# Kernel tuning notes

Measured on AMD Instinct MI355X. Metric: run time of the kernel, lower is better.

The kernel has to match this reference:

```python
import jax, jax.numpy as jnp
import numpy as np

NUM_HEADS = 8
HIDDEN_DIM = 256
QUERY_DIM = 256
HEAD_DIM = HIDDEN_DIM // NUM_HEADS
NORM_FACT = float(HIDDEN_DIM / NUM_HEADS) ** (-0.5)


def setup_inputs() -> dict:
    key = jax.random.key(0)
    k1, k2, k3, k4, k5 = jax.random.split(key, 5)
    B, Q, H, W = 16, 100, 64, 64
    q = jax.random.normal(k1, (B, Q, QUERY_DIM), dtype=jnp.float32)
    k = jax.random.normal(k2, (B, QUERY_DIM, H, W), dtype=jnp.float32)
    mask = jax.random.randint(k3, (B, H, W), 0, 2).astype(jnp.bool_)
    # xavier_uniform for [hidden, query] linear weights
    limit = float(np.sqrt(6.0 / (HIDDEN_DIM + QUERY_DIM)))
    Wq = jax.random.uniform(k4, (HIDDEN_DIM, QUERY_DIM), minval=-limit, maxval=limit, dtype=jnp.float32)
    Wk = jax.random.uniform(k5, (HIDDEN_DIM, QUERY_DIM), minval=-limit, maxval=limit, dtype=jnp.float32)
    bq = jnp.zeros((HIDDEN_DIM,), dtype=jnp.float32)
    bk = jnp.zeros((HIDDEN_DIM,), dtype=jnp.float32)
    return {"q": q, "k": k, "Wq": Wq, "bq": bq, "Wk": Wk, "bk": bk, "mask": mask}


def reference(q, k, Wq, bq, Wk, bk, mask):
    B, Q, _ = q.shape
    _, C, H, W = k.shape
    # q projection: [B, Q, hidden]
    qp = jnp.einsum('bqc,hc->bqh', q, Wq) + bq
    # k projection via 1x1 conv == channelwise linear: [B, hidden, H, W]
    kp = jnp.einsum('bchw,oc->bohw', k, Wk) + bk[None, :, None, None]
    # split heads: qh [B,Q,nh,hd], kh [B,nh,hd,H,W]
    qh = qp.reshape(B, Q, NUM_HEADS, HEAD_DIM)
    kh = kp.reshape(B, NUM_HEADS, HEAD_DIM, H, W)
    # scores [B,Q,nh,H,W]
    weights = jnp.einsum('bqnd,bndhw->bqnhw', qh, kh) * NORM_FACT
    # masked fill: mask [B,H,W] -> broadcast over (Q, heads)
    weights = jnp.where(mask[:, None, None, :, :], -jnp.inf, weights)
    # softmax jointly over (heads, H, W), as in torch flatten(2)
    flat = weights.reshape(B, Q, NUM_HEADS * H * W)
    flat = jax.nn.softmax(flat, axis=-1)
    return flat.reshape(B, Q, NUM_HEADS, H, W)
```

## Files before the change

kernel.cpp:

```cpp
#include <hip/hip_runtime.h>
#include <hip/hip_bf16.h>
#include <math.h>

#define BB 16
#define QQ 100
#define NH 8
#define HWN 4096
#define NORM_FACT 0.17677669529663687f
#define QPAD 112

typedef short bf16x8_t __attribute__((ext_vector_type(8)));
typedef float f32x4_t  __attribute__((ext_vector_type(4)));

__device__ __forceinline__ unsigned short bf16bits(float f) {
    __hip_bfloat16 h = __float2bfloat16(f);
    return __builtin_bit_cast(unsigned short, h);
}
__device__ __forceinline__ float bf16tof(unsigned short u) {
    union { unsigned int i; float f; } x; x.i = (unsigned int)u << 16; return x.f;
}

__global__ void k_prep(const float* __restrict__ Wq, const float* __restrict__ Wk,
                       float* __restrict__ WqT, unsigned short* __restrict__ Wkbf) {
    int idx = blockIdx.x;
    int h = threadIdx.x;
    if (idx < 256) {
        WqT[idx * 256 + h] = Wq[h * 256 + idx];
    } else {
        int r = idx - 256;
        Wkbf[r * 256 + h] = bf16bits(Wk[r * 256 + h]);
    }
}

__global__ __launch_bounds__(256) void k_qproj(const float* __restrict__ q,
                                               const float* __restrict__ WqT,
                                               const float* __restrict__ bq,
                                               unsigned short* __restrict__ qphi,
                                               unsigned short* __restrict__ qplo) {
    int blk = blockIdx.x;
    int b = blk / 28, q0 = (blk % 28) * 4;
    int h = threadIdx.x;
    size_t obase = ((size_t)b * QPAD + q0) * 256 + h;
    if (q0 >= QQ) {
#pragma unroll
        for (int i = 0; i < 4; ++i) { qphi[obase + i * 256] = 0; qplo[obase + i * 256] = 0; }
        return;
    }
    __shared__ float qsh[4][256];
    int ibase = (b * QQ + q0) * 256;
#pragma unroll
    for (int i = 0; i < 4; ++i) qsh[i][h] = q[ibase + i * 256 + h];
    __syncthreads();
    float bias = bq[h];
    float a0 = bias, a1 = bias, a2 = bias, a3 = bias;
    for (int c = 0; c < 256; ++c) {
        float wv = WqT[c * 256 + h];
        a0 = fmaf(qsh[0][c], wv, a0);
        a1 = fmaf(qsh[1][c], wv, a1);
        a2 = fmaf(qsh[2][c], wv, a2);
        a3 = fmaf(qsh[3][c], wv, a3);
    }
    float a[4] = {a0 * NORM_FACT, a1 * NORM_FACT, a2 * NORM_FACT, a3 * NORM_FACT};
#pragma unroll
    for (int i = 0; i < 4; ++i) {
        unsigned short hi = bf16bits(a[i]);
        qphi[obase + i * 256] = hi;
        qplo[obase + i * 256] = bf16bits(a[i] - bf16tof(hi));
    }
}

__global__ __launch_bounds__(512) void k_kproj3(const float* __restrict__ k,
                                                const unsigned short* __restrict__ Wkbf,
                                                const float* __restrict__ bk,
                                                unsigned short* __restrict__ kpT) {
    int b = blockIdx.y;
    int hwblk = blockIdx.x * 64;
    int t = threadIdx.x;
    int w = t >> 6, lane = t & 63;
    int hwt = w & 3, oh = w >> 2;
    int n15 = lane & 15, kg = lane >> 4;
    int hw_l = hwt * 16 + n15;

    __shared__ float lds_f[64][140];

    f32x4_t acc[8];
#pragma unroll
    for (int m = 0; m < 8; ++m) acc[m] = f32x4_t{0.f, 0.f, 0.f, 0.f};

    const float* kb = k + (size_t)b * 256 * HWN + hwblk;
    const unsigned short* wbase = Wkbf + ((size_t)(oh * 128 + n15)) * 256 + kg * 8;
    int c_l = t >> 4, l16 = t & 15;

#pragma unroll
    for (int chunk = 0; chunk < 2; ++chunk) {
#pragma unroll
        for (int p = 0; p < 4; ++p) {
            int cc = p * 32 + c_l;
            float4 v = *(const float4*)(kb + (size_t)(chunk * 128 + cc) * HWN + l16 * 4);
            lds_f[l16 * 4 + 0][cc] = v.x;
            lds_f[l16 * 4 + 1][cc] = v.y;
            lds_f[l16 * 4 + 2][cc] = v.z;
            lds_f[l16 * 4 + 3][cc] = v.w;
        }
        __syncthreads();
#pragma unroll
        for (int ksl = 0; ksl < 4; ++ksl) {
            f32x4_t f0 = *(const f32x4_t*)&lds_f[hw_l][ksl * 32 + kg * 8];
            f32x4_t f1 = *(const f32x4_t*)&lds_f[hw_l][ksl * 32 + kg * 8 + 4];
            bf16x8_t bfrag;
#pragma unroll
            for (int j = 0; j < 4; ++j) {
                bfrag[j]     = (short)bf16bits(f0[j]);
                bfrag[4 + j] = (short)bf16bits(f1[j]);
            }
            int ks = chunk * 4 + ksl;
#pragma unroll
            for (int m = 0; m < 8; ++m) {
                bf16x8_t afrag = *reinterpret_cast<const bf16x8_t*>(wbase + (size_t)m * 16 * 256 + ks * 32);
                acc[m] = __builtin_amdgcn_mfma_f32_16x16x32_bf16(afrag, bfrag, acc[m], 0, 0, 0);
            }
        }
        __syncthreads();
    }

    unsigned short* tile2 = (unsigned short*)lds_f;
#pragma unroll
    for (int m = 0; m < 8; ++m) {
        ushort4 pk;
        unsigned short* pkp = (unsigned short*)&pk;
#pragma unroll
        for (int r = 0; r < 4; ++r) {
            int o = oh * 128 + m * 16 + kg * 4 + r;
            pkp[r] = bf16bits(acc[m][r] + bk[o]);
        }
        *(ushort4*)&tile2[(size_t)hw_l * 264 + oh * 128 + m * 16 + kg * 4] = pk;
    }
    __syncthreads();
    int l5 = t & 31;
#pragma unroll
    for (int it = 0; it < 4; ++it) {
        int row = it * 16 + (t >> 5);
        uint4 v = *(const uint4*)&tile2[(size_t)row * 264 + l5 * 8];
        *(uint4*)(kpT + ((size_t)b * HWN + hwblk + row) * 256 + l5 * 8) = v;
    }
}

__global__ __launch_bounds__(256) void k_sums(const unsigned short* __restrict__ qphi,
                                              const unsigned short* __restrict__ qplo,
                                              const unsigned short* __restrict__ kpT,
                                              const int* __restrict__ mask,
                                              float* __restrict__ partial) {
    int hwb = blockIdx.x, b = blockIdx.y;
    int t = threadIdx.x, w = t >> 6, lane = t & 63;
    int n15 = lane & 15, kg = lane >> 4;
    int hw = hwb * 64 + w * 16 + n15;
    float mm = mask[b * HWN + hw] ? 0.0f : 1.0f;

    __shared__ float ldsbuf[8960];
    unsigned short* sA = (unsigned short*)ldsbuf;

    const unsigned short* brow = kpT + ((size_t)(b * HWN + hw)) * 256 + kg * 8;
    bf16x8_t bfr[8];
#pragma unroll
    for (int n = 0; n < NH; ++n)
        bfr[n] = *reinterpret_cast<const bf16x8_t*>(brow + n * 32);

    const unsigned short* ghi = qphi + (size_t)b * QPAD * 256;
    const unsigned short* glo = qplo + (size_t)b * QPAD * 256;
    int srow = t >> 4, schunk = t & 15;

    float sums[7][4] = {};
#pragma unroll 1
    for (int mt = 0; mt < 7; ++mt) {
        const unsigned short* shi = ghi + (size_t)(mt * 16 + srow) * 256 + schunk * 16;
        const unsigned short* slo = glo + (size_t)(mt * 16 + srow) * 256 + schunk * 16;
        uint4 vhi0 = *(const uint4*)(shi);
        uint4 vhi1 = *(const uint4*)(shi + 8);
        uint4 vlo0 = *(const uint4*)(slo);
        uint4 vlo1 = *(const uint4*)(slo + 8);
        *(uint4*)&sA[srow * 264 + schunk * 16]          = vhi0;
        *(uint4*)&sA[srow * 264 + schunk * 16 + 8]      = vhi1;
        *(uint4*)&sA[16 * 264 + srow * 264 + schunk * 16]     = vlo0;
        *(uint4*)&sA[16 * 264 + srow * 264 + schunk * 16 + 8] = vlo1;
        __syncthreads();
#pragma unroll
        for (int n = 0; n < NH; ++n) {
            bf16x8_t ahi = *reinterpret_cast<const bf16x8_t*>(&sA[n15 * 264 + n * 32 + kg * 8]);
            bf16x8_t alo = *reinterpret_cast<const bf16x8_t*>(&sA[16 * 264 + n15 * 264 + n * 32 + kg * 8]);
            f32x4_t a2 = {0.f, 0.f, 0.f, 0.f};
            a2 = __builtin_amdgcn_mfma_f32_16x16x32_bf16(ahi, bfr[n], a2, 0, 0, 0);
            a2 = __builtin_amdgcn_mfma_f32_16x16x32_bf16(alo, bfr[n], a2, 0, 0, 0);
#pragma unroll
            for (int r = 0; r < 4; ++r)
                sums[mt][r] += __expf(a2[r]) * mm;
        }
        __syncthreads();
    }

    float* R = ldsbuf + w * 112 * 20;
#pragma unroll
    for (int mt = 0; mt < 7; ++mt)
#pragma unroll
        for (int r = 0; r < 4; ++r)
            R[(mt * 16 + kg * 4 + r) * 20 + n15] = sums[mt][r];
    if (lane < 56) {
#pragma unroll
        for (int p = 0; p < 2; ++p) {
            int row = lane + p * 56;
            f32x4_t v0 = *(const f32x4_t*)&R[row * 20 + 0];
            f32x4_t v1 = *(const f32x4_t*)&R[row * 20 + 4];
            f32x4_t v2 = *(const f32x4_t*)&R[row * 20 + 8];
            f32x4_t v3 = *(const f32x4_t*)&R[row * 20 + 12];
            float s = (v0[0]+v0[1]+v0[2]+v0[3]) + (v1[0]+v1[1]+v1[2]+v1[3])
                    + (v2[0]+v2[1]+v2[2]+v2[3]) + (v3[0]+v3[1]+v3[2]+v3[3]);
            partial[((size_t)b * QPAD + row) * 256 + hwb * 4 + w] = s;
        }
    }
}

__global__ __launch_bounds__(256) void k_invsum(const float* __restrict__ partial,
                                                float* __restrict__ inv) {
    int blk = blockIdx.x;
    int b = blk / QQ, qq = blk % QQ;
    const float* p = partial + ((size_t)b * QPAD + qq) * 256;
    int t = threadIdx.x;
    float v = p[t];
#pragma unroll
    for (int off = 32; off; off >>= 1) v += __shfl_xor(v, off, 64);
    __shared__ float red[4];
    if ((t & 63) == 0) red[t >> 6] = v;
    __syncthreads();
    if (t == 0) inv[blk] = 1.0f / (red[0] + red[1] + red[2] + red[3]);
}

__global__ __launch_bounds__(256) void k_write(const unsigned short* __restrict__ qphi,
                                               const unsigned short* __restrict__ qplo,
                                               const unsigned short* __restrict__ kpT,
                                               const int* __restrict__ mask,
                                               const float* __restrict__ inv,
                                               float* __restrict__ out) {
    int qt = blockIdx.x, n = blockIdx.y, b = blockIdx.z;
    int t = threadIdx.x, w = t >> 6, lane = t & 63;
    int n15 = lane & 15, kg = lane >> 4;

    bf16x8_t ahi = *reinterpret_cast<const bf16x8_t*>(
        qphi + ((size_t)(b * QPAD + qt * 16 + n15)) * 256 + n * 32 + kg * 8);
    bf16x8_t alo = *reinterpret_cast<const bf16x8_t*>(
        qplo + ((size_t)(b * QPAD + qt * 16 + n15)) * 256 + n * 32 + kg * 8);
    float invq[4];
#pragma unroll
    for (int r = 0; r < 4; ++r) {
        int qrow = qt * 16 + kg * 4 + r;
        invq[r] = (qrow < QQ) ? inv[b * QQ + qrow] : 0.0f;
    }

    __shared__ float lt[16][260];

    bf16x8_t bc[4], bn[4];
    float mc[4], mn[4];
#pragma unroll
    for (int ht = 0; ht < 4; ++ht) {
        int hw = w * 64 + ht * 16 + n15;
        bc[ht] = *reinterpret_cast<const bf16x8_t*>(
            kpT + ((size_t)(b * HWN + hw)) * 256 + n * 32 + kg * 8);
        mc[ht] = mask[b * HWN + hw] ? 0.0f : 1.0f;
        bn[ht] = bc[ht];
        mn[ht] = mc[ht];
    }

#pragma unroll 1
    for (int hws = 0; hws < 16; ++hws) {
        if (hws < 15) {
#pragma unroll
            for (int ht = 0; ht < 4; ++ht) {
                int hw = (hws + 1) * 256 + w * 64 + ht * 16 + n15;
                bn[ht] = *reinterpret_cast<const bf16x8_t*>(
                    kpT + ((size_t)(b * HWN + hw)) * 256 + n * 32 + kg * 8);
                mn[ht] = mask[b * HWN + hw] ? 0.0f : 1.0f;
            }
        }
#pragma unroll
        for (int ht = 0; ht < 4; ++ht) {
            f32x4_t acc = {0.f, 0.f, 0.f, 0.f};
            acc = __builtin_amdgcn_mfma_f32_16x16x32_bf16(ahi, bc[ht], acc, 0, 0, 0);
            acc = __builtin_amdgcn_mfma_f32_16x16x32_bf16(alo, bc[ht], acc, 0, 0, 0);
#pragma unroll
            for (int r = 0; r < 4; ++r)
                lt[kg * 4 + r][w * 64 + ht * 16 + n15] = __expf(acc[r]) * mc[ht] * invq[r];
        }
        __syncthreads();
#pragma unroll
        for (int j = 0; j < 4; ++j) {
            int row = w * 4 + j;
            int qrow = qt * 16 + row;
            f32x4_t v4 = *(const f32x4_t*)&lt[row][lane * 4];
            if (qrow < QQ)
                __builtin_nontemporal_store(v4,
                    (f32x4_t*)(out + (((size_t)(b * QQ + qrow)) * NH + n) * HWN + hws * 256 + lane * 4));
        }
        __syncthreads();
#pragma unroll
        for (int ht = 0; ht < 4; ++ht) { bc[ht] = bn[ht]; mc[ht] = mn[ht]; }
    }
}

extern "C" void kernel_launch(void* const* d_in, const int* in_sizes, int n_in,
                              void* d_out, int out_size, void* d_ws, size_t ws_size,
                              hipStream_t stream) {
    const float* q    = (const float*)d_in[0];
    const float* k    = (const float*)d_in[1];
    const float* Wq   = (const float*)d_in[2];
    const float* bq   = (const float*)d_in[3];
    const float* Wk   = (const float*)d_in[4];
    const float* bk   = (const float*)d_in[5];
    const int*   mask = (const int*)d_in[6];
    float* out = (float*)d_out;

    char* base = (char*)d_ws;
    unsigned short* kpT  = (unsigned short*)(base);
    unsigned short* qphi = (unsigned short*)(base + 33554432);
    unsigned short* qplo = (unsigned short*)(base + 34471936);
    float*  WqT     = (float*)(base + 35389440);
    unsigned short* Wkbf = (unsigned short*)(base + 35651584);
    float*  partial = (float*)(base + 35782656);
    float*  inv     = (float*)(base + 37617664);
    if (ws_size < (size_t)37624064) return;

    k_prep  <<<dim3(512), dim3(256), 0, stream>>>(Wq, Wk, WqT, Wkbf);
    k_qproj <<<dim3(448), dim3(256), 0, stream>>>(q, WqT, bq, qphi, qplo);
    k_kproj3<<<dim3(64, 16), dim3(512), 0, stream>>>(k, Wkbf, bk, kpT);
    k_sums  <<<dim3(64, 16), dim3(256), 0, stream>>>(qphi, qplo, kpT, mask, partial);
    k_invsum<<<dim3(1600), dim3(256), 0, stream>>>(partial, inv);
    k_write <<<dim3(7, 8, 16), dim3(256), 0, stream>>>(qphi, qplo, kpT, mask, inv, out);
}
```

Baseline: 192.9 us.

## Store projected keys in MFMA-fragment-major layout and shrink kproj LDS footprint

The key projection output is now written in a fragment-ordered layout (batch, 16-row tile, head, k-group, lane) so that each wave in k_sums and k_write loads its bf16x8 B-fragments as contiguous 16-byte chunks rather than strided 512-byte rows. The kproj kernel also halves its LDS staging buffer by processing four 64-channel chunks instead of two 128-channel chunks and writing out each 128-output half in turn. This aims to coalesce the key reads in the two consumer kernels and to raise kproj occupancy, at the cost of extra barriers and a non-unrolled chunk loop in kproj.

```diff
diff --git a/kernel.cpp b/kernel.cpp
--- a/kernel.cpp
+++ b/kernel.cpp
@@ -8,6 +8,8 @@
 #define HWN 4096
 #define NORM_FACT 0.17677669529663687f
 #define QPAD 112
+
+#define KPF_IDX(b, tile, n, kg) (((((size_t)(b) * 256 + (tile)) * 8 + (n)) * 4 + (kg)) * 128)
 
 typedef short bf16x8_t __attribute__((ext_vector_type(8)));
 typedef float f32x4_t  __attribute__((ext_vector_type(4)));
@@ -69,10 +71,10 @@
     }
 }
 
-__global__ __launch_bounds__(512) void k_kproj3(const float* __restrict__ k,
+__global__ __launch_bounds__(512) void k_kproj4(const float* __restrict__ k,
                                                 const unsigned short* __restrict__ Wkbf,
                                                 const float* __restrict__ bk,
-                                                unsigned short* __restrict__ kpT) {
+                                                unsigned short* __restrict__ kpf) {
     int b = blockIdx.y;
     int hwblk = blockIdx.x * 64;
     int t = threadIdx.x;
@@ -81,7 +83,7 @@
     int n15 = lane & 15, kg = lane >> 4;
     int hw_l = hwt * 16 + n15;
 
-    __shared__ float lds_f[64][140];
+    __shared__ float lds_f[64][68];
 
     f32x4_t acc[8];
 #pragma unroll
@@ -91,12 +93,12 @@
     const unsigned short* wbase = Wkbf + ((size_t)(oh * 128 + n15)) * 256 + kg * 8;
     int c_l = t >> 4, l16 = t & 15;
 
-#pragma unroll
-    for (int chunk = 0; chunk < 2; ++chunk) {
-#pragma unroll
-        for (int p = 0; p < 4; ++p) {
+#pragma unroll 1
+    for (int chunk = 0; chunk < 4; ++chunk) {
+#pragma unroll
+        for (int p = 0; p < 2; ++p) {
             int cc = p * 32 + c_l;
-            float4 v = *(const float4*)(kb + (size_t)(chunk * 128 + cc) * HWN + l16 * 4);
+            float4 v = *(const float4*)(kb + (size_t)(chunk * 64 + cc) * HWN + l16 * 4);
             lds_f[l16 * 4 + 0][cc] = v.x;
             lds_f[l16 * 4 + 1][cc] = v.y;
             lds_f[l16 * 4 + 2][cc] = v.z;
@@ -104,7 +106,7 @@
         }
         __syncthreads();
 #pragma unroll
-        for (int ksl = 0; ksl < 4; ++ksl) {
+        for (int ksl = 0; ksl < 2; ++ksl) {
             f32x4_t f0 = *(const f32x4_t*)&lds_f[hw_l][ksl * 32 + kg * 8];
             f32x4_t f1 = *(const f32x4_t*)&lds_f[hw_l][ksl * 32 + kg * 8 + 4];
             bf16x8_t bfrag;
@@ -113,7 +115,7 @@
                 bfrag[j]     = (short)bf16bits(f0[j]);
                 bfrag[4 + j] = (short)bf16bits(f1[j]);
             }
-            int ks = chunk * 4 + ksl;
+            int ks = chunk * 2 + ksl;
 #pragma unroll
             for (int m = 0; m < 8; ++m) {
                 bf16x8_t afrag = *reinterpret_cast<const bf16x8_t*>(wbase + (size_t)m * 16 * 256 + ks * 32);
@@ -124,30 +126,42 @@
     }
 
     unsigned short* tile2 = (unsigned short*)lds_f;
-#pragma unroll
-    for (int m = 0; m < 8; ++m) {
-        ushort4 pk;
-        unsigned short* pkp = (unsigned short*)&pk;
-#pragma unroll
-        for (int r = 0; r < 4; ++r) {
-            int o = oh * 128 + m * 16 + kg * 4 + r;
-            pkp[r] = bf16bits(acc[m][r] + bk[o]);
-        }
-        *(ushort4*)&tile2[(size_t)hw_l * 264 + oh * 128 + m * 16 + kg * 4] = pk;
-    }
-    __syncthreads();
-    int l5 = t & 31;
-#pragma unroll
-    for (int it = 0; it < 4; ++it) {
-        int row = it * 16 + (t >> 5);
-        uint4 v = *(const uint4*)&tile2[(size_t)row * 264 + l5 * 8];
-        *(uint4*)(kpT + ((size_t)b * HWN + hwblk + row) * 256 + l5 * 8) = v;
+#pragma unroll 1
+    for (int ohp = 0; ohp < 2; ++ohp) {
+        if (oh == ohp) {
+#pragma unroll
+            for (int m = 0; m < 8; ++m) {
+                ushort4 pk;
+                unsigned short* pkp = (unsigned short*)&pk;
+#pragma unroll
+                for (int r = 0; r < 4; ++r) {
+                    int o = ohp * 128 + m * 16 + kg * 4 + r;
+                    pkp[r] = bf16bits(acc[m][r] + bk[o]);
+                }
+                *(ushort4*)&tile2[(size_t)hw_l * 132 + m * 16 + kg * 4] = pk;
+            }
+        }
+        __syncthreads();
+        {
+            int s = t * 2;
+            int tile = s >> 8;
+            int n2   = (s >> 6) & 3;
+            int kgc  = (s >> 4) & 3;
+            int nl   = s & 15;
+            const unsigned short* src = &tile2[(size_t)(tile * 16 + nl) * 132 + n2 * 32 + kgc * 8];
+            uint4 v0 = *(const uint4*)(src);
+            uint4 v1 = *(const uint4*)(src + 132);
+            size_t dst = KPF_IDX(b, blockIdx.x * 4 + tile, ohp * 4 + n2, kgc) + nl * 8;
+            *(uint4*)(kpf + dst)     = v0;
+            *(uint4*)(kpf + dst + 8) = v1;
+        }
+        __syncthreads();
     }
 }
 
 __global__ __launch_bounds__(256) void k_sums(const unsigned short* __restrict__ qphi,
                                               const unsigned short* __restrict__ qplo,
-                                              const unsigned short* __restrict__ kpT,
+                                              const unsigned short* __restrict__ kpf,
                                               const int* __restrict__ mask,
                                               float* __restrict__ partial) {
     int hwb = blockIdx.x, b = blockIdx.y;
@@ -159,11 +173,11 @@
     __shared__ float ldsbuf[8960];
     unsigned short* sA = (unsigned short*)ldsbuf;
 
-    const unsigned short* brow = kpT + ((size_t)(b * HWN + hw)) * 256 + kg * 8;
+    int tg = hwb * 4 + w;
     bf16x8_t bfr[8];
 #pragma unroll
     for (int n = 0; n < NH; ++n)
-        bfr[n] = *reinterpret_cast<const bf16x8_t*>(brow + n * 32);
+        bfr[n] = *reinterpret_cast<const bf16x8_t*>(kpf + KPF_IDX(b, tg, n, kg) + n15 * 8);
 
     const unsigned short* ghi = qphi + (size_t)b * QPAD * 256;
     const unsigned short* glo = qplo + (size_t)b * QPAD * 256;
@@ -235,7 +249,7 @@
 
 __global__ __launch_bounds__(256) void k_write(const unsigned short* __restrict__ qphi,
                                                const unsigned short* __restrict__ qplo,
-                                               const unsigned short* __restrict__ kpT,
+                                               const unsigned short* __restrict__ kpf,
                                                const int* __restrict__ mask,
                                                const float* __restrict__ inv,
                                                float* __restrict__ out) {
@@ -260,10 +274,9 @@
     float mc[4], mn[4];
 #pragma unroll
     for (int ht = 0; ht < 4; ++ht) {
-        int hw = w * 64 + ht * 16 + n15;
-        bc[ht] = *reinterpret_cast<const bf16x8_t*>(
-            kpT + ((size_t)(b * HWN + hw)) * 256 + n * 32 + kg * 8);
-        mc[ht] = mask[b * HWN + hw] ? 0.0f : 1.0f;
+        int tg = w * 4 + ht;
+        bc[ht] = *reinterpret_cast<const bf16x8_t*>(kpf + KPF_IDX(b, tg, n, kg) + n15 * 8);
+        mc[ht] = mask[b * HWN + w * 64 + ht * 16 + n15] ? 0.0f : 1.0f;
         bn[ht] = bc[ht];
         mn[ht] = mc[ht];
     }
@@ -273,10 +286,9 @@
         if (hws < 15) {
 #pragma unroll
             for (int ht = 0; ht < 4; ++ht) {
-                int hw = (hws + 1) * 256 + w * 64 + ht * 16 + n15;
-                bn[ht] = *reinterpret_cast<const bf16x8_t*>(
-                    kpT + ((size_t)(b * HWN + hw)) * 256 + n * 32 + kg * 8);
-                mn[ht] = mask[b * HWN + hw] ? 0.0f : 1.0f;
+                int tg = (hws + 1) * 16 + w * 4 + ht;
+                bn[ht] = *reinterpret_cast<const bf16x8_t*>(kpf + KPF_IDX(b, tg, n, kg) + n15 * 8);
+                mn[ht] = mask[b * HWN + (hws + 1) * 256 + w * 64 + ht * 16 + n15] ? 0.0f : 1.0f;
             }
         }
 #pragma unroll
@@ -317,7 +329,7 @@
     float* out = (float*)d_out;
 
     char* base = (char*)d_ws;
-    unsigned short* kpT  = (unsigned short*)(base);
+    unsigned short* kpf  = (unsigned short*)(base);
     unsigned short* qphi = (unsigned short*)(base + 33554432);
     unsigned short* qplo = (unsigned short*)(base + 34471936);
     float*  WqT     = (float*)(base + 35389440);
@@ -328,8 +340,8 @@
 
     k_prep  <<<dim3(512), dim3(256), 0, stream>>>(Wq, Wk, WqT, Wkbf);
     k_qproj <<<dim3(448), dim3(256), 0, stream>>>(q, WqT, bq, qphi, qplo);
-    k_kproj3<<<dim3(64, 16), dim3(512), 0, stream>>>(k, Wkbf, bk, kpT);
-    k_sums  <<<dim3(64, 16), dim3(256), 0, stream>>>(qphi, qplo, kpT, mask, partial);
+    k_kproj4<<<dim3(64, 16), dim3(512), 0, stream>>>(k, Wkbf, bk, kpf);
+    k_sums  <<<dim3(64, 16), dim3(256), 0, stream>>>(qphi, qplo, kpf, mask, partial);
     k_invsum<<<dim3(1600), dim3(256), 0, stream>>>(partial, inv);
-    k_write <<<dim3(7, 8, 16), dim3(256), 0, stream>>>(qphi, qplo, kpT, mask, inv, out);
-}
+    k_write <<<dim3(7, 8, 16), dim3(256), 0, stream>>>(qphi, qplo, kpf, mask, inv, out);
+}
```

New measurement: 186.5 us. -3.3%, faster.
